# Kernel tuning notes

Hardware: AMD Instinct MI355X
Metric: run time of the kernel (lower is better)

Reference implementation:

```python
import jax, jax.numpy as jnp
import numpy as np

A = 15           # anchors per location (5 sizes x 3 ratios)
H, W = 200, 320  # feature map size
N = 8            # batch
STRIDE = 4
PRE_NMS = 2000
POST_NMS = 1000
NMS_THRESH = 0.7
MIN_SIZE = 1.0
SCORE_THRESH = 0.0
BBOX_CLIP = float(np.log(1000.0 / 16.0))  # torchvision BoxCoder clamp on dw/dh


def _make_anchors():
    # torchvision-style cell anchors: ratio-major, then sizes, shifted over the grid.
    sizes = np.array([32.0, 64.0, 128.0, 256.0, 512.0])
    ratios = np.array([0.5, 1.0, 2.0])
    h_r = np.sqrt(ratios)
    w_r = 1.0 / h_r
    ws = (w_r[:, None] * sizes[None, :]).reshape(-1)  # [15]
    hs = (h_r[:, None] * sizes[None, :]).reshape(-1)
    base = np.stack([-ws, -hs, ws, hs], axis=1) / 2.0  # [15,4] centered at 0
    sx = np.arange(W) * STRIDE
    sy = np.arange(H) * STRIDE
    yy, xx = np.meshgrid(sy, sx, indexing="ij")
    shifts = np.stack([xx, yy, xx, yy], axis=-1).reshape(-1, 1, 4)  # [H*W,1,4]
    return (shifts + base[None]).reshape(-1, 4).astype(np.float32)  # [H*W*A,4]


def setup_inputs() -> dict:
    key = jax.random.key(0)
    k1, k2 = jax.random.split(key)
    return {
        "box_cls": jax.random.normal(k1, (N, A, H, W), dtype=jnp.float32),
        "box_regression": jax.random.normal(k2, (N, 4 * A, H, W), dtype=jnp.float32),
        "anchors": jnp.asarray(_make_anchors()),
        "img_h": 800,
        "img_w": 1280,
    }


def _decode(deltas, anchors):
    # BoxCoder.decode with weights (1,1,1,1). deltas [N,K,4], anchors [K,4] xyxy.
    wa = anchors[:, 2] - anchors[:, 0]
    ha = anchors[:, 3] - anchors[:, 1]
    cxa = anchors[:, 0] + 0.5 * wa
    cya = anchors[:, 1] + 0.5 * ha
    dx, dy = deltas[..., 0], deltas[..., 1]
    dw = jnp.minimum(deltas[..., 2], BBOX_CLIP)
    dh = jnp.minimum(deltas[..., 3], BBOX_CLIP)
    cx = dx * wa + cxa
    cy = dy * ha + cya
    w = wa * jnp.exp(dw)
    h = ha * jnp.exp(dh)
    return jnp.stack(
        [cx - 0.5 * w, cy - 0.5 * h, cx + 0.5 * w, cy + 0.5 * h], axis=-1
    )


def _nms_keep(boxes, scores):
    # Greedy NMS over boxes sorted by descending score; scores < 0 mark invalid.
    x1, y1, x2, y2 = boxes[:, 0], boxes[:, 1], boxes[:, 2], boxes[:, 3]
    area = (x2 - x1) * (y2 - y1)
    ix = jnp.maximum(0.0, jnp.minimum(x2[:, None], x2[None, :]) - jnp.maximum(x1[:, None], x1[None, :]))
    iy = jnp.maximum(0.0, jnp.minimum(y2[:, None], y2[None, :]) - jnp.maximum(y1[:, None], y1[None, :]))
    inter = ix * iy
    iou = inter / (area[:, None] + area[None, :] - inter)  # [K,K]
    k = boxes.shape[0]
    idx = jnp.arange(k)
    keep0 = scores >= 0.0

    def body(i, keep):
        sup = keep[i] & (iou[i] > NMS_THRESH) & (idx > i)
        return keep & ~sup

    return jax.lax.fori_loop(0, k, body, keep0)


def reference(box_cls, box_regression, anchors, img_h, img_w):
    n = box_cls.shape[0]
    # permute_and_flatten: [N, A*C, H, W] -> [N, H*W*A, C]
    objectness = box_cls.reshape(n, A, 1, H, W).transpose(0, 3, 4, 1, 2).reshape(n, -1)
    deltas = box_regression.reshape(n, A, 4, H, W).transpose(0, 3, 4, 1, 2).reshape(n, -1, 4)
    proposals = _decode(deltas, anchors)  # [N, K, 4]
    # clip to image (single image size for the whole batch)
    fh = jnp.float32(img_h)
    fw = jnp.float32(img_w)
    proposals = jnp.stack(
        [
            jnp.clip(proposals[..., 0], 0.0, fw),
            jnp.clip(proposals[..., 1], 0.0, fh),
            jnp.clip(proposals[..., 2], 0.0, fw),
            jnp.clip(proposals[..., 3], 0.0, fh),
        ],
        axis=-1,
    )
    # pre-NMS top-k per image (single feature level)
    top_s, top_i = jax.lax.top_k(objectness, PRE_NMS)        # [N, PRE]
    boxes = jnp.take_along_axis(proposals, top_i[..., None], axis=1)  # [N, PRE, 4]
    scores = jax.nn.sigmoid(top_s)
    # remove small boxes and low-scoring boxes (mask instead of dynamic shapes)
    ws = boxes[..., 2] - boxes[..., 0]
    hs = boxes[..., 3] - boxes[..., 1]
    valid = (ws >= MIN_SIZE) & (hs >= MIN_SIZE) & (scores >= SCORE_THRESH)
    scores_m = jnp.where(valid, scores, -1.0)
    order = jnp.argsort(-scores_m, axis=1)
    boxes_s = jnp.take_along_axis(boxes, order[..., None], axis=1)
    scores_s = jnp.take_along_axis(scores_m, order, axis=1)
    keep = jax.vmap(_nms_keep)(boxes_s, scores_s)            # [N, PRE] bool
    ks = jnp.where(keep, scores_s, -1.0)
    fs, fi = jax.lax.top_k(ks, POST_NMS)                     # [N, POST]
    fb = jnp.take_along_axis(boxes_s, fi[..., None], axis=1)
    ok = fs >= 0.0
    final_boxes = jnp.where(ok[..., None], fb, 0.0)          # zero-padded, fixed shape
    final_scores = jnp.where(ok, fs, 0.0)
    return final_boxes, final_scores
```

## Files before the change

### kernel.cpp

```cpp
#include <hip/hip_runtime.h>
#include <hip/hip_bf16.h>
#include <stdint.h>

typedef unsigned long long u64;

#define AN 15
#define HH 200
#define WW 320
#define HWSZ (HH*WW)
#define PER (AN*HWSZ)
#define NB 8
#define K_PRE 2000
#define K_POST 1000
#define SORTN 4096
#define HBINS 4096
#define HBLK 64
#define CBLK 16
#define SLICE (SORTN/CBLK)
#define NMS_TH 0.7f
#define BBOX_CLIP_F 4.135166556742356f
#define FLOOR12 3072u
#define SENT 0xFFFFFFFFu

#define PHI(x) ((x) + ((x) >> 3))

__device__ __forceinline__ unsigned keyOfU(unsigned u) {
    return (u & 0x80000000u) ? ~u : (u | 0x80000000u);
}
__device__ __forceinline__ float valOf(unsigned k) {
    unsigned u = (k & 0x80000000u) ? (k ^ 0x80000000u) : ~k;
    return __uint_as_float(u);
}

__global__ __launch_bounds__(256)
void z_init(uint4* __restrict__ gh4, unsigned* __restrict__ selT12) {
    gh4[blockIdx.x * 256 + threadIdx.x] = make_uint4(0, 0, 0, 0);
    if (blockIdx.x == 0 && threadIdx.x < NB) selT12[threadIdx.x] = SENT;
}

__global__ __launch_bounds__(256)
void k_histF(const uint4* __restrict__ cls4, unsigned* __restrict__ gh) {
    int n = blockIdx.y;
    __shared__ unsigned lh[HBINS];
    for (int b = threadIdx.x; b < HBINS; b += 256) lh[b] = 0;
    __syncthreads();
    const uint4* p = cls4 + (size_t)n * (PER / 4);
    int stride = gridDim.x * 256;
    int i = blockIdx.x * 256 + threadIdx.x;
#define H4(vv) { unsigned k0 = keyOfU((vv).x) >> 20, k1 = keyOfU((vv).y) >> 20, \
                          k2 = keyOfU((vv).z) >> 20, k3 = keyOfU((vv).w) >> 20; \
        if (k0 >= FLOOR12) atomicAdd(&lh[k0], 1u);                              \
        if (k1 >= FLOOR12) atomicAdd(&lh[k1], 1u);                              \
        if (k2 >= FLOOR12) atomicAdd(&lh[k2], 1u);                              \
        if (k3 >= FLOOR12) atomicAdd(&lh[k3], 1u); }
    for (; i + stride < PER / 4; i += 2 * stride) {
        uint4 a = p[i];
        uint4 b = p[i + stride];
        H4(a) H4(b)
    }
    if (i < PER / 4) { uint4 a = p[i]; H4(a) }
#undef H4
    __syncthreads();
    unsigned* dst = gh + (size_t)n * HBINS;
    for (int b = threadIdx.x; b < HBINS; b += 256) {
        unsigned v = lh[b];
        if (v) atomicAdd(&dst[b], v);
    }
}

__global__ __launch_bounds__(1024)
void k_sel(const unsigned* __restrict__ gh, unsigned* __restrict__ selT12) {
    int n = blockIdx.x, t = threadIdx.x;
    __shared__ unsigned L[1024];
    uint4 v = *(const uint4*)(gh + (size_t)n * HBINS + 4 * t);
    unsigned sf[5];
    sf[3] = v.w; sf[2] = v.z + sf[3]; sf[1] = v.y + sf[2]; sf[0] = v.x + sf[1];
    L[t] = sf[0];
    __syncthreads();
    for (int off = 1; off < 1024; off <<= 1) {
        unsigned x = L[t] + ((t + off < 1024) ? L[t + off] : 0u);
        __syncthreads(); L[t] = x; __syncthreads();
    }
    unsigned tail = (t < 1023) ? L[t + 1] : 0u;
    sf[0] += tail; sf[1] += tail; sf[2] += tail; sf[3] += tail; sf[4] = tail;
#pragma unroll
    for (int e = 0; e < 4; ++e)
        if (sf[e] >= K_PRE && sf[e + 1] < K_PRE) selT12[n] = 4u * t + e;
}

__global__ __launch_bounds__(256)
void k_histR(const uint4* __restrict__ cls4, unsigned* __restrict__ gh,
             const unsigned* __restrict__ selT12) {
    int n = blockIdx.y;
    if (selT12[n] != SENT) return;
    __shared__ unsigned lh[HBINS];
    for (int b = threadIdx.x; b < HBINS; b += 256) lh[b] = 0;
    __syncthreads();
    const uint4* p = cls4 + (size_t)n * (PER / 4);
    int stride = gridDim.x * 256;
#define H4(vv) { unsigned k0 = keyOfU((vv).x) >> 20, k1 = keyOfU((vv).y) >> 20, \
                          k2 = keyOfU((vv).z) >> 20, k3 = keyOfU((vv).w) >> 20; \
        if (k0 < FLOOR12) atomicAdd(&lh[k0], 1u);                               \
        if (k1 < FLOOR12) atomicAdd(&lh[k1], 1u);                               \
        if (k2 < FLOOR12) atomicAdd(&lh[k2], 1u);                               \
        if (k3 < FLOOR12) atomicAdd(&lh[k3], 1u); }
    for (int i = blockIdx.x * 256 + threadIdx.x; i < PER / 4; i += stride) {
        uint4 a = p[i]; H4(a)
    }
#undef H4
    __syncthreads();
    unsigned* dst = gh + (size_t)n * HBINS;
    for (int b = threadIdx.x; b < HBINS; b += 256) {
        unsigned v = lh[b];
        if (v) atomicAdd(&dst[b], v);
    }
}

__global__ __launch_bounds__(1024)
void k_selR(const unsigned* __restrict__ gh, unsigned* __restrict__ selT12) {
    int n = blockIdx.x, t = threadIdx.x;
    if (selT12[n] != SENT) return;
    __shared__ unsigned L[1024];
    uint4 v = *(const uint4*)(gh + (size_t)n * HBINS + 4 * t);
    unsigned sf[5];
    sf[3] = v.w; sf[2] = v.z + sf[3]; sf[1] = v.y + sf[2]; sf[0] = v.x + sf[1];
    L[t] = sf[0];
    __syncthreads();
    for (int off = 1; off < 1024; off <<= 1) {
        unsigned x = L[t] + ((t + off < 1024) ? L[t + off] : 0u);
        __syncthreads(); L[t] = x; __syncthreads();
    }
    unsigned tail = (t < 1023) ? L[t + 1] : 0u;
    sf[0] += tail; sf[1] += tail; sf[2] += tail; sf[3] += tail; sf[4] = tail;
#pragma unroll
    for (int e = 0; e < 4; ++e)
        if (sf[e] >= K_PRE && sf[e + 1] < K_PRE) selT12[n] = 4u * t + e;
}

__global__ __launch_bounds__(512)
void k_compact(const uint4* __restrict__ cls4, const unsigned* __restrict__ selT12,
               u64* __restrict__ cand) {
    int n = blockIdx.y;
    unsigned t12 = selT12[n];
    __shared__ unsigned cnt;
    if (threadIdx.x == 0) cnt = 0;
    __syncthreads();
    u64* slice = cand + (size_t)n * SORTN + (size_t)blockIdx.x * SLICE;
    const uint4* p = cls4 + (size_t)n * (PER / 4);
    int stride = gridDim.x * 512;

#define PROC(vv, ii) {                                                        \
        unsigned kk[4] = {keyOfU((vv).x), keyOfU((vv).y), keyOfU((vv).z),     \
                          keyOfU((vv).w)};                                    \
        int i0 = (ii) * 4;                                                    \
        int a = i0 / HWSZ;                                                    \
        int r0 = i0 - a * HWSZ;                                               \
        _Pragma("unroll")                                                     \
        for (int c = 0; c < 4; ++c) {                                         \
            if ((kk[c] >> 20) >= t12) {                                       \
                unsigned pos = atomicAdd(&cnt, 1u);                           \
                if (pos < SLICE) {                                            \
                    unsigned idx = (unsigned)((r0 + c) * AN + a);             \
                    slice[pos] = ((u64)kk[c] << 32) | (u64)(~idx);            \
                }                                                             \
            }                                                                 \
        }                                                                     \
    }

    int i = blockIdx.x * 512 + threadIdx.x;
    for (; i + 3 * stride < PER / 4; i += 4 * stride) {
        uint4 v0 = p[i];
        uint4 v1 = p[i + stride];
        uint4 v2 = p[i + 2 * stride];
        uint4 v3 = p[i + 3 * stride];
        PROC(v0, i) PROC(v1, i + stride) PROC(v2, i + 2 * stride) PROC(v3, i + 3 * stride)
    }
    for (; i < PER / 4; i += stride) { uint4 v0 = p[i]; PROC(v0, i) }
#undef PROC

    __syncthreads();
    unsigned c0 = cnt; if (c0 > SLICE) c0 = SLICE;
    for (unsigned t = c0 + threadIdx.x; t < SLICE; t += 512) slice[t] = 0ull;
}

__global__ __launch_bounds__(512)
void k_sort(u64* __restrict__ cand) {
    int n = blockIdx.x;
    int tid = threadIdx.x;
    __shared__ u64 sb[PHI(SORTN - 1) + 1];
    u64 r[8];

#define CE(a_, b_, d_) { bool sw_ = (d_) ? (r[a_] < r[b_]) : (r[a_] > r[b_]); \
                         if (sw_) { u64 t_ = r[a_]; r[a_] = r[b_]; r[b_] = t_; } }

    {
        const u64* src = cand + (size_t)n * SORTN + 8 * tid;
#pragma unroll
        for (int e = 0; e < 8; ++e) r[e] = src[e];
        CE(0, 1, true)  CE(2, 3, false) CE(4, 5, true)  CE(6, 7, false)
        CE(0, 2, true)  CE(1, 3, true)  CE(4, 6, false) CE(5, 7, false)
        CE(0, 1, true)  CE(2, 3, true)  CE(4, 5, false) CE(6, 7, false)
#pragma unroll
        for (int e = 0; e < 8; ++e) sb[9 * tid + e] = r[e];
        __syncthreads();
    }

    for (int k = 8; k <= SORTN; k <<= 1) {
        for (int j = k >> 1; j >= 8; j >>= 1) {
#pragma unroll
            for (int s = 0; s < 4; ++s) {
                int c = tid + s * 512;
                int i = ((c & ~(j - 1)) << 1) | (c & (j - 1));
                int p = i | j;
                bool dir = (i & k) == 0;
                u64 a = sb[PHI(i)], b = sb[PHI(p)];
                bool sw = dir ? (a < b) : (a > b);
                if (sw) { sb[PHI(i)] = b; sb[PHI(p)] = a; }
            }
            __syncthreads();
        }
        {
            bool d = ((8 * tid) & k) == 0;
#pragma unroll
            for (int e = 0; e < 8; ++e) r[e] = sb[9 * tid + e];
            CE(0, 4, d) CE(1, 5, d) CE(2, 6, d) CE(3, 7, d)
            CE(0, 2, d) CE(1, 3, d) CE(4, 6, d) CE(5, 7, d)
            CE(0, 1, d) CE(2, 3, d) CE(4, 5, d) CE(6, 7, d)
#pragma unroll
            for (int e = 0; e < 8; ++e) sb[9 * tid + e] = r[e];
            __syncthreads();
        }
    }
#undef CE

    for (int t = tid; t < 2048; t += 512)
        cand[(size_t)n * SORTN + t] = sb[PHI(t)];
}

__global__ __launch_bounds__(1024)
void k_decode(const float* __restrict__ reg, const float* __restrict__ anchors,
              const int* __restrict__ pih, const int* __restrict__ piw,
              const u64* __restrict__ cand,
              float* __restrict__ boxes_s, float* __restrict__ scores_s) {
    int n = blockIdx.x;
    int tid = threadIdx.x;
    float fh = (float)(*pih);
    float fw = (float)(*piw);

    float bx[2][4]; float sc[2]; int pred[2];
#pragma unroll
    for (int q = 0; q < 2; ++q) {
        int t = tid + 1024 * q;
        pred[q] = 0; sc[q] = -1.0f;
        bx[q][0] = bx[q][1] = bx[q][2] = bx[q][3] = 0.f;
        if (t < K_PRE) {
            u64 e = cand[(size_t)n * SORTN + t];
            unsigned key = (unsigned)(e >> 32);
            unsigned idx = ~((unsigned)e);
            float v = valOf(key);
            float s = 1.0f / (1.0f + expf(-v));
            int a = (int)(idx % AN);
            int rr = (int)(idx / AN);
            size_t base = ((size_t)(n * AN + a) * 4) * HWSZ + rr;
            float dx = reg[base];
            float dy = reg[base + HWSZ];
            float dw = reg[base + 2 * (size_t)HWSZ];
            float dh = reg[base + 3 * (size_t)HWSZ];
            float4 an4 = ((const float4*)anchors)[idx];
            float wa = an4.z - an4.x, ha = an4.w - an4.y;
            float cxa = an4.x + 0.5f * wa, cya = an4.y + 0.5f * ha;
            dw = fminf(dw, BBOX_CLIP_F); dh = fminf(dh, BBOX_CLIP_F);
            float cx = dx * wa + cxa, cy = dy * ha + cya;
            float w = wa * expf(dw), h = ha * expf(dh);
            float x1 = cx - 0.5f * w, y1 = cy - 0.5f * h;
            float x2 = cx + 0.5f * w, y2 = cy + 0.5f * h;
            x1 = fminf(fmaxf(x1, 0.f), fw);
            y1 = fminf(fmaxf(y1, 0.f), fh);
            x2 = fminf(fmaxf(x2, 0.f), fw);
            y2 = fminf(fmaxf(y2, 0.f), fh);
            bool valid = ((x2 - x1) >= 1.0f) && ((y2 - y1) >= 1.0f);
            bx[q][0] = x1; bx[q][1] = y1; bx[q][2] = x2; bx[q][3] = y2;
            sc[q] = s; pred[q] = valid ? 1 : 0;
        }
    }

    __shared__ u64 ww[32];
    __shared__ int wpfx[33];
    int lane = tid & 63, wid = tid >> 6;
#pragma unroll
    for (int q = 0; q < 2; ++q) {
        u64 bal = __ballot(pred[q] != 0);
        if (lane == 0) ww[wid + 16 * q] = bal;
    }
    __syncthreads();
    if (tid == 0) {
        int s = 0;
#pragma unroll
        for (int w2 = 0; w2 < 32; ++w2) { wpfx[w2] = s; s += (int)__popcll(ww[w2]); }
        wpfx[32] = s;
    }
    __syncthreads();
    int V = wpfx[32];

#pragma unroll
    for (int q = 0; q < 2; ++q) {
        int t = tid + 1024 * q;
        if (t < K_PRE) {
            int wi = t >> 6;
            int before = wpfx[wi] + (int)__popcll(ww[wi] & ((1ull << (unsigned)lane) - 1ull));
            int pos = pred[q] ? before : (V + (t - before));
            float4 b4; b4.x = bx[q][0]; b4.y = bx[q][1]; b4.z = bx[q][2]; b4.w = bx[q][3];
            ((float4*)boxes_s)[(size_t)n * K_PRE + pos] = b4;
            scores_s[(size_t)n * K_PRE + pos] = pred[q] ? sc[q] : -1.0f;
        }
    }
}

__global__ __launch_bounds__(64)
void k_maskT(const float* __restrict__ boxes_s, u64* __restrict__ maskT) {
    int n = blockIdx.y;
    int p = blockIdx.x;
    int lane = threadIdx.x;
    int cb = (int)((sqrtf(8.0f * (float)p + 1.0f) - 1.0f) * 0.5f);
    while ((cb + 1) * (cb + 2) / 2 <= p) ++cb;
    while (cb * (cb + 1) / 2 > p) --cb;
    int rb = p - cb * (cb + 1) / 2;

    __shared__ float rx1[64], ry1[64], rx2[64], ry2[64], rar[64];
    int c = cb * 64 + lane;
    bool cok = c < K_PRE;
    float4 c4; c4.x = c4.y = c4.z = c4.w = 0.f;
    if (cok) c4 = ((const float4*)boxes_s)[(size_t)n * K_PRE + c];
    float areaC = (c4.z - c4.x) * (c4.w - c4.y);

    int r = rb * 64 + lane;
    float4 r4; r4.x = r4.y = r4.z = r4.w = 0.f;
    if (r < K_PRE) r4 = ((const float4*)boxes_s)[(size_t)n * K_PRE + r];
    rx1[lane] = r4.x; ry1[lane] = r4.y; rx2[lane] = r4.z; ry2[lane] = r4.w;
    rar[lane] = (r4.z - r4.x) * (r4.w - r4.y);
    __syncthreads();

    u64 bits = 0;
    int bmax = 0;
    if (cok) { bmax = c - rb * 64; if (bmax > 64) bmax = 64; }
    for (int b = 0; b < bmax; ++b) {
        float ix = fminf(c4.z, rx2[b]) - fmaxf(c4.x, rx1[b]); ix = fmaxf(ix, 0.f);
        float iy = fminf(c4.w, ry2[b]) - fmaxf(c4.y, ry1[b]); iy = fmaxf(iy, 0.f);
        float inter = ix * iy;
        float iou = inter / (rar[b] + areaC - inter);
        if (iou > NMS_TH) bits |= (1ull << b);
    }
    maskT[((size_t)n * 32 + rb) * 2048 + c] = bits;
}

__global__ __launch_bounds__(64)
void k_scanT(const u64* __restrict__ maskT, const float* __restrict__ boxes_s,
             const float* __restrict__ scores_s, float* __restrict__ out) {
    int n = blockIdx.x;
    int lane = threadIdx.x;
    __shared__ float ls[2048];
    __shared__ u64 keptw[32];
    for (int i = lane; i < 512; i += 64)
        ((float4*)ls)[i] = ((const float4*)(scores_s + (size_t)n * K_PRE))[i];
    if (lane < 48) ls[2000 + lane] = -1.0f;
    if (lane < 32) keptw[lane] = 0ull;
    __syncthreads();

    const u64* mb = maskT + (size_t)n * 32 * 2048;
    int kept_total = 0;

    u64 wv[32];
#pragma unroll
    for (int rb = 0; rb < 32; ++rb) wv[rb] = mb[(size_t)rb * 2048 + lane];

    for (int f = 0; f < 32; ++f) {
        int c = f * 64 + lane;

        u64 wn[32];
        if (f < 31) {
            int cn = c + 64;
#pragma unroll
            for (int rb = 0; rb < 32; ++rb) wn[rb] = mb[(size_t)rb * 2048 + cn];
        }

        u64 hit = 0;
#pragma unroll
        for (int rb = 0; rb < 32; ++rb) hit |= (wv[rb] & keptw[rb]);
        bool ext = hit != 0ull;
        u64 diag = wv[f];

        bool v = (ls[c] >= 0.0f) && !ext;
        u64 kept = __ballot(v);
        while (true) {
            u64 nk = __ballot(v && ((diag & kept) == 0ull));
            if (nk == kept) break;
            kept = nk;
        }

        if ((kept >> lane) & 1ull) {
            int rank = kept_total + (int)__popcll(kept & ((1ull << lane) - 1ull));
            if (rank < K_POST) {
                float4 b4 = ((const float4*)boxes_s)[(size_t)n * K_PRE + c];
                ((float4*)out)[(size_t)n * K_POST + rank] = b4;
                out[(size_t)NB * K_POST * 4 + (size_t)n * K_POST + rank] = ls[c];
            }
        }
        kept_total += (int)__popcll(kept);
        if (lane == 0) keptw[f] = kept;
        if (kept_total >= K_POST || f == 31) break;
#pragma unroll
        for (int rb = 0; rb < 32; ++rb) wv[rb] = wn[rb];
    }

    int start = (kept_total < K_POST) ? kept_total : K_POST;
    float4 z4; z4.x = z4.y = z4.z = z4.w = 0.f;
    for (int rk = start + lane; rk < K_POST; rk += 64) {
        ((float4*)out)[(size_t)n * K_POST + rk] = z4;
        out[(size_t)NB * K_POST * 4 + (size_t)n * K_POST + rk] = 0.f;
    }
}

extern "C" void kernel_launch(void* const* d_in, const int* in_sizes, int n_in,
                              void* d_out, int out_size, void* d_ws, size_t ws_size,
                              hipStream_t stream) {
    const float* cls     = (const float*)d_in[0];
    const float* regr    = (const float*)d_in[1];
    const float* anchors = (const float*)d_in[2];
    const int*   pih     = (const int*)d_in[3];
    const int*   piw     = (const int*)d_in[4];
    float* out = (float*)d_out;

    char* w = (char*)d_ws;
    u64*      maskT   = (u64*)(w + 0);
    unsigned* gh      = (unsigned*)(w + 4194304);
    unsigned* selT12  = (unsigned*)(w + 4325376);
    u64*      cand    = (u64*)(w + 4325408);
    float*    boxes_s = (float*)(w + 4587552);
    float*    scores_s= (float*)(w + 4843552);

    z_init<<<32, 256, 0, stream>>>((uint4*)gh, selT12);
    k_histF<<<dim3(HBLK, NB), 256, 0, stream>>>((const uint4*)cls, gh);
    k_sel<<<NB, 1024, 0, stream>>>(gh, selT12);
    k_histR<<<dim3(HBLK, NB), 256, 0, stream>>>((const uint4*)cls, gh, selT12);
    k_selR<<<NB, 1024, 0, stream>>>(gh, selT12);
    k_compact<<<dim3(CBLK, NB), 512, 0, stream>>>((const uint4*)cls, selT12, cand);
    k_sort<<<NB, 512, 0, stream>>>(cand);
    k_decode<<<NB, 1024, 0, stream>>>(regr, anchors, pih, piw,
                                      cand, boxes_s, scores_s);
    k_maskT<<<dim3(528, NB), 64, 0, stream>>>(boxes_s, maskT);
    k_scanT<<<NB, 64, 0, stream>>>(maskT, boxes_s, scores_s, out);
    (void)in_sizes; (void)n_in; (void)ws_size;
}
```

Measured before the change: 127.4 us.

## Fuse candidate compaction into histogram pass and filter from per-block buffers

```diff
diff --git a/kernel.cpp b/kernel.cpp
--- a/kernel.cpp
+++ b/kernel.cpp
@@ -15,6 +15,7 @@
 #define SORTN 4096
 #define HBINS 4096
 #define HBLK 64
+#define FSLICE 512
 #define CBLK 16
 #define SLICE (SORTN/CBLK)
 #define NMS_TH 0.7f
@@ -39,28 +40,50 @@
 }
 
 __global__ __launch_bounds__(256)
-void k_histF(const uint4* __restrict__ cls4, unsigned* __restrict__ gh) {
+void k_hc(const uint4* __restrict__ cls4, unsigned* __restrict__ gh,
+          u64* __restrict__ fbuf) {
     int n = blockIdx.y;
     __shared__ unsigned lh[HBINS];
+    __shared__ unsigned cnt;
     for (int b = threadIdx.x; b < HBINS; b += 256) lh[b] = 0;
-    __syncthreads();
+    if (threadIdx.x == 0) cnt = 0;
+    __syncthreads();
+    u64* slice = fbuf + ((size_t)n * HBLK + blockIdx.x) * FSLICE;
     const uint4* p = cls4 + (size_t)n * (PER / 4);
     int stride = gridDim.x * 256;
+
+#define PROC(vv, ii) {                                                        \
+        unsigned kk[4] = {keyOfU((vv).x), keyOfU((vv).y), keyOfU((vv).z),     \
+                          keyOfU((vv).w)};                                    \
+        int i0 = (ii) * 4;                                                    \
+        int a = i0 / HWSZ;                                                    \
+        int r0 = i0 - a * HWSZ;                                               \
+        _Pragma("unroll")                                                     \
+        for (int c = 0; c < 4; ++c) {                                         \
+            unsigned k12 = kk[c] >> 20;                                       \
+            if (k12 >= FLOOR12) {                                             \
+                atomicAdd(&lh[k12], 1u);                                      \
+                unsigned pos = atomicAdd(&cnt, 1u);                           \
+                if (pos < FSLICE) {                                           \
+                    unsigned idx = (unsigned)((r0 + c) * AN + a);             \
+                    slice[pos] = ((u64)kk[c] << 32) | (u64)(~idx);            \
+                }                                                             \
+            }                                                                 \
+        }                                                                     \
+    }
+
     int i = blockIdx.x * 256 + threadIdx.x;
-#define H4(vv) { unsigned k0 = keyOfU((vv).x) >> 20, k1 = keyOfU((vv).y) >> 20, \
-                          k2 = keyOfU((vv).z) >> 20, k3 = keyOfU((vv).w) >> 20; \
-        if (k0 >= FLOOR12) atomicAdd(&lh[k0], 1u);                              \
-        if (k1 >= FLOOR12) atomicAdd(&lh[k1], 1u);                              \
-        if (k2 >= FLOOR12) atomicAdd(&lh[k2], 1u);                              \
-        if (k3 >= FLOOR12) atomicAdd(&lh[k3], 1u); }
     for (; i + stride < PER / 4; i += 2 * stride) {
-        uint4 a = p[i];
-        uint4 b = p[i + stride];
-        H4(a) H4(b)
-    }
-    if (i < PER / 4) { uint4 a = p[i]; H4(a) }
-#undef H4
-    __syncthreads();
+        uint4 a4 = p[i];
+        uint4 b4 = p[i + stride];
+        PROC(a4, i) PROC(b4, i + stride)
+    }
+    if (i < PER / 4) { uint4 a4 = p[i]; PROC(a4, i) }
+#undef PROC
+
+    __syncthreads();
+    unsigned c0 = cnt; if (c0 > FSLICE) c0 = FSLICE;
+    for (unsigned t = c0 + threadIdx.x; t < FSLICE; t += 256) slice[t] = 0ull;
     unsigned* dst = gh + (size_t)n * HBINS;
     for (int b = threadIdx.x; b < HBINS; b += 256) {
         unsigned v = lh[b];
@@ -137,50 +160,49 @@
         if (sf[e] >= K_PRE && sf[e + 1] < K_PRE) selT12[n] = 4u * t + e;
 }
 
-__global__ __launch_bounds__(512)
-void k_compact(const uint4* __restrict__ cls4, const unsigned* __restrict__ selT12,
-               u64* __restrict__ cand) {
-    int n = blockIdx.y;
+__global__ __launch_bounds__(256)
+void k_filter(const uint4* __restrict__ cls4, const u64* __restrict__ fbuf,
+              const unsigned* __restrict__ selT12, u64* __restrict__ cand) {
+    int n = blockIdx.y, cb = blockIdx.x;
     unsigned t12 = selT12[n];
     __shared__ unsigned cnt;
     if (threadIdx.x == 0) cnt = 0;
     __syncthreads();
-    u64* slice = cand + (size_t)n * SORTN + (size_t)blockIdx.x * SLICE;
-    const uint4* p = cls4 + (size_t)n * (PER / 4);
-    int stride = gridDim.x * 512;
-
-#define PROC(vv, ii) {                                                        \
-        unsigned kk[4] = {keyOfU((vv).x), keyOfU((vv).y), keyOfU((vv).z),     \
-                          keyOfU((vv).w)};                                    \
-        int i0 = (ii) * 4;                                                    \
-        int a = i0 / HWSZ;                                                    \
-        int r0 = i0 - a * HWSZ;                                               \
-        _Pragma("unroll")                                                     \
-        for (int c = 0; c < 4; ++c) {                                         \
-            if ((kk[c] >> 20) >= t12) {                                       \
-                unsigned pos = atomicAdd(&cnt, 1u);                           \
-                if (pos < SLICE) {                                            \
-                    unsigned idx = (unsigned)((r0 + c) * AN + a);             \
-                    slice[pos] = ((u64)kk[c] << 32) | (u64)(~idx);            \
-                }                                                             \
-            }                                                                 \
-        }                                                                     \
-    }
-
-    int i = blockIdx.x * 512 + threadIdx.x;
-    for (; i + 3 * stride < PER / 4; i += 4 * stride) {
-        uint4 v0 = p[i];
-        uint4 v1 = p[i + stride];
-        uint4 v2 = p[i + 2 * stride];
-        uint4 v3 = p[i + 3 * stride];
-        PROC(v0, i) PROC(v1, i + stride) PROC(v2, i + 2 * stride) PROC(v3, i + 3 * stride)
-    }
-    for (; i < PER / 4; i += stride) { uint4 v0 = p[i]; PROC(v0, i) }
-#undef PROC
-
+    u64* slice = cand + (size_t)n * SORTN + (size_t)cb * SLICE;
+
+    if (t12 >= FLOOR12) {
+        const u64* src = fbuf + ((size_t)n * HBLK + (size_t)cb * (HBLK / CBLK)) * FSLICE;
+        for (int t = threadIdx.x; t < (HBLK / CBLK) * FSLICE; t += 256) {
+            u64 e = src[t];
+            if ((unsigned)(e >> 52) >= t12) {
+                unsigned pos = atomicAdd(&cnt, 1u);
+                if (pos < SLICE) slice[pos] = e;
+            }
+        }
+    } else {
+        const uint4* p = cls4 + (size_t)n * (PER / 4);
+        int stride = gridDim.x * 256;
+        for (int i = cb * 256 + threadIdx.x; i < PER / 4; i += stride) {
+            uint4 v = p[i];
+            unsigned kk[4] = {keyOfU(v.x), keyOfU(v.y), keyOfU(v.z), keyOfU(v.w)};
+            int i0 = i * 4;
+            int a = i0 / HWSZ;
+            int r0 = i0 - a * HWSZ;
+#pragma unroll
+            for (int c = 0; c < 4; ++c) {
+                if ((kk[c] >> 20) >= t12) {
+                    unsigned pos = atomicAdd(&cnt, 1u);
+                    if (pos < SLICE) {
+                        unsigned idx = (unsigned)((r0 + c) * AN + a);
+                        slice[pos] = ((u64)kk[c] << 32) | (u64)(~idx);
+                    }
+                }
+            }
+        }
+    }
     __syncthreads();
     unsigned c0 = cnt; if (c0 > SLICE) c0 = SLICE;
-    for (unsigned t = c0 + threadIdx.x; t < SLICE; t += 512) slice[t] = 0ull;
+    for (unsigned t = c0 + threadIdx.x; t < SLICE; t += 256) slice[t] = 0ull;
 }
 
 __global__ __launch_bounds__(512)
@@ -360,7 +382,7 @@
     int lane = threadIdx.x;
     __shared__ float ls[2048];
     __shared__ u64 keptw[32];
-    for (int i = lane; i < 512; i += 64)
+    for (int i = lane; i < 500; i += 64)
         ((float4*)ls)[i] = ((const float4*)(scores_s + (size_t)n * K_PRE))[i];
     if (lane < 48) ls[2000 + lane] = -1.0f;
     if (lane < 32) keptw[lane] = 0ull;
@@ -434,16 +456,17 @@
     u64*      maskT   = (u64*)(w + 0);
     unsigned* gh      = (unsigned*)(w + 4194304);
     unsigned* selT12  = (unsigned*)(w + 4325376);
-    u64*      cand    = (u64*)(w + 4325408);
-    float*    boxes_s = (float*)(w + 4587552);
-    float*    scores_s= (float*)(w + 4843552);
+    u64*      cand    = (u64*)(w + 4325440);
+    float*    boxes_s = (float*)(w + 4587584);
+    float*    scores_s= (float*)(w + 4843584);
+    u64*      fbuf    = (u64*)(w + 4907584);
 
     z_init<<<32, 256, 0, stream>>>((uint4*)gh, selT12);
-    k_histF<<<dim3(HBLK, NB), 256, 0, stream>>>((const uint4*)cls, gh);
+    k_hc<<<dim3(HBLK, NB), 256, 0, stream>>>((const uint4*)cls, gh, fbuf);
     k_sel<<<NB, 1024, 0, stream>>>(gh, selT12);
     k_histR<<<dim3(HBLK, NB), 256, 0, stream>>>((const uint4*)cls, gh, selT12);
     k_selR<<<NB, 1024, 0, stream>>>(gh, selT12);
-    k_compact<<<dim3(CBLK, NB), 512, 0, stream>>>((const uint4*)cls, selT12, cand);
+    k_filter<<<dim3(CBLK, NB), 256, 0, stream>>>((const uint4*)cls, fbuf, selT12, cand);
     k_sort<<<NB, 512, 0, stream>>>(cand);
     k_decode<<<NB, 1024, 0, stream>>>(regr, anchors, pih, piw,
                                       cand, boxes_s, scores_s);
```

Result: no change. 126.4 us (-0.8%).
